# Performance work log

Hardware: AMD Instinct MI355X
Metric: run time of the kernel (lower is better)

Reference implementation:

```python
import jax, jax.numpy as jnp
import numpy as np

B, N, E, C_IN, C_OUT, N_LAYERS = 4, 20000, 16, 128, 128, 3


def setup_inputs() -> dict:
    key = jax.random.key(0)
    kx, ke, k0, k1, k2 = jax.random.split(key, 5)
    x = jax.random.normal(kx, (B, N, C_IN), dtype=jnp.float32)
    # neighbor lists padded with -1 (as in the torch module)
    edge_index = jax.random.randint(ke, (B, N, E), -1, N, dtype=jnp.int32)
    s_in = 1.0 / np.sqrt(C_IN)
    s_out = 1.0 / np.sqrt(C_OUT)
    W0 = jax.random.uniform(k0, (C_OUT, C_IN), minval=-s_in, maxval=s_in, dtype=jnp.float32)
    W1 = jax.random.uniform(k1, (C_OUT, C_OUT), minval=-s_out, maxval=s_out, dtype=jnp.float32)
    W2 = jax.random.uniform(k2, (C_OUT, C_OUT), minval=-s_out, maxval=s_out, dtype=jnp.float32)
    return {"x": x, "edge_index": edge_index, "W0": W0, "W1": W1, "W2": W2}


def gcn_layer(x, edge_index, W):
    # x: [B, N, Cin], edge_index: [B, N, E] (pad = -1), W: [Cout, Cin]
    n_nodes = x.shape[1]
    deg = jnp.sum(edge_index >= 0, axis=-1, keepdims=True).astype(x.dtype) + 1.0  # [B,N,1]
    inv_sqrt_deg = 1.0 / jnp.sqrt(deg)
    h = jnp.einsum('bnc,oc->bno', x, W) * inv_sqrt_deg  # transform + 1/sqrt(deg)
    # padding row of zeros at index n_nodes; map -1 -> n_nodes
    padded = jnp.concatenate(
        [h, jnp.zeros((h.shape[0], 1, h.shape[2]), h.dtype)], axis=1)  # [B,N+1,Cout]
    idx = jnp.where(edge_index < 0, n_nodes, edge_index)
    neigh = jax.vmap(lambda p, e: p[e])(padded, idx)  # [B,N,E,Cout] gather
    # sum over neighbors + self, then scale again by 1/sqrt(deg)
    return (jnp.sum(neigh, axis=-2) + h) * inv_sqrt_deg


def reference(x, edge_index, W0, W1, W2):
    for W in (W0, W1, W2):
        x = jax.nn.elu(gcn_layer(x, edge_index, W))
    return x
```

## Files before the change

### kernel.cpp

```cpp
#include <hip/hip_runtime.h>
#include <hip/hip_bf16.h>

#define NB 4
#define NN 20000
#define NE 16
#define NC 128
#define M_TOTAL (NB * NN)
#define BM 64

typedef __attribute__((ext_vector_type(8))) short bf16x8;
typedef __attribute__((ext_vector_type(4))) short short4v;
typedef __attribute__((ext_vector_type(4))) float f32x4;

static __device__ __forceinline__ short f2bf(float x) {
    __hip_bfloat16 h = __float2bfloat16(x);
    return *reinterpret_cast<short*>(&h);
}
static __device__ __forceinline__ float bf2f(short s) {
    __hip_bfloat16 h = *reinterpret_cast<__hip_bfloat16*>(&s);
    return __bfloat162float(h);
}

__global__ __launch_bounds__(256) void isd_kernel(const int* __restrict__ ei,
                                                  float* __restrict__ isd) {
    int g = blockIdx.x * 256 + threadIdx.x;
    if (g >= M_TOTAL) return;
    const int4* e4 = (const int4*)(ei + (size_t)g * NE);
    int cnt = 1;
#pragma unroll
    for (int q = 0; q < 4; ++q) {
        int4 v = e4[q];
        cnt += (v.x >= 0) + (v.y >= 0) + (v.z >= 0) + (v.w >= 0);
    }
    isd[g] = 1.0f / sqrtf((float)cnt);
}

__global__ __launch_bounds__(256) void wpack_kernel(const float* __restrict__ W,
                                                    short* __restrict__ wp) {
    const int id = blockIdx.x * 256 + threadIdx.x;
    const int s = id >> 9;
    const int f = (id >> 6) & 7;
    const int l = id & 63;
    const int o = f * 16 + (l & 15);
    const int kb = s * 32 + (l >> 4) * 8;
    const float4 v0 = *(const float4*)(W + (size_t)o * NC + kb);
    const float4 v1 = *(const float4*)(W + (size_t)o * NC + kb + 4);
    const float xs[8] = {v0.x, v0.y, v0.z, v0.w, v1.x, v1.y, v1.z, v1.w};
    bf16x8 hv, lv;
#pragma unroll
    for (int e = 0; e < 8; ++e) {
        const short h = f2bf(xs[e]);
        hv[e] = h;
        lv[e] = f2bf(xs[e] - bf2f(h));
    }
    short* dst = wp + (size_t)((s * 8 + f) * 2) * 512 + l * 8;
    *(bf16x8*)dst = hv;
    *(bf16x8*)(dst + 512) = lv;
}

__global__ __launch_bounds__(256) void matmul_kernel(const float* __restrict__ X,
                                                     const short* __restrict__ wp,
                                                     const float* __restrict__ isd,
                                                     float* __restrict__ H) {
    __shared__ short Ah[64 * 128];
    __shared__ short Al[64 * 128];
    const int t = threadIdx.x;
    const int bm = blockIdx.x * BM;

#pragma unroll
    for (int j = 0; j < 8; ++j) {
        const int fi = j * 256 + t;
        const int row = fi >> 5;
        const int k0 = (t & 31) * 4;
        const float4 v = *(const float4*)(X + (size_t)bm * NC + (size_t)fi * 4);
        const float xs[4] = {v.x, v.y, v.z, v.w};
        short4v hi, lo;
#pragma unroll
        for (int e = 0; e < 4; ++e) {
            const short h = f2bf(xs[e]);
            hi[e] = h;
            lo[e] = f2bf(xs[e] - bf2f(h));
        }
        const int kblk = k0 >> 3;
        const int dst = row * 128 + ((kblk ^ (row & 7)) << 3) + (k0 & 7);
        *(short4v*)(Ah + dst) = hi;
        *(short4v*)(Al + dst) = lo;
    }
    __syncthreads();

    const int w = t >> 6, l = t & 63;
    const int m0 = (w >> 1) * 32;
    const int oh = w & 1;
    const int lr = l & 15, lg = l >> 4;

    f32x4 acc[2][4];
#pragma unroll
    for (int mf = 0; mf < 2; ++mf)
#pragma unroll
        for (int fi = 0; fi < 4; ++fi) acc[mf][fi] = (f32x4){0.f, 0.f, 0.f, 0.f};

#pragma unroll
    for (int s = 0; s < 4; ++s) {
        bf16x8 a_h[2], a_l[2], b_h[4], b_l[4];
#pragma unroll
        for (int fi = 0; fi < 4; ++fi) {
            const int fg = oh * 4 + fi;
            const short* ph = wp + (size_t)((s * 8 + fg) * 2) * 512 + l * 8;
            b_h[fi] = *(const bf16x8*)ph;
            b_l[fi] = *(const bf16x8*)(ph + 512);
        }
#pragma unroll
        for (int mf = 0; mf < 2; ++mf) {
            const int row = m0 + mf * 16 + lr;
            const int kblk = (s * 4 + lg) ^ (l & 7);
            a_h[mf] = *(const bf16x8*)(Ah + row * 128 + kblk * 8);
            a_l[mf] = *(const bf16x8*)(Al + row * 128 + kblk * 8);
        }
#pragma unroll
        for (int mf = 0; mf < 2; ++mf)
#pragma unroll
            for (int fi = 0; fi < 4; ++fi) {
                acc[mf][fi] = __builtin_amdgcn_mfma_f32_16x16x32_bf16(
                    a_l[mf], b_h[fi], acc[mf][fi], 0, 0, 0);
                acc[mf][fi] = __builtin_amdgcn_mfma_f32_16x16x32_bf16(
                    a_h[mf], b_l[fi], acc[mf][fi], 0, 0, 0);
                acc[mf][fi] = __builtin_amdgcn_mfma_f32_16x16x32_bf16(
                    a_h[mf], b_h[fi], acc[mf][fi], 0, 0, 0);
            }
    }

#pragma unroll
    for (int mf = 0; mf < 2; ++mf)
#pragma unroll
        for (int r = 0; r < 4; ++r) {
            const int m = bm + m0 + mf * 16 + lg * 4 + r;
            const float sd = isd[m];
#pragma unroll
            for (int fi = 0; fi < 4; ++fi)
                H[(size_t)m * NC + oh * 64 + fi * 16 + lr] = acc[mf][fi][r] * sd;
        }
}

__global__ __launch_bounds__(256) void gather_kernel(const float* __restrict__ H,
                                                     const int* __restrict__ ei,
                                                     const float* __restrict__ isd,
                                                     float* __restrict__ out) {
    const int wid = threadIdx.x >> 6;
    const int lane = threadIdx.x & 63;
    int g = blockIdx.x * 4 + wid;
    g = __builtin_amdgcn_readfirstlane(g);
    const int base = (g / NN) * NN;

    const int4* e4 = (const int4*)(ei + (size_t)g * NE);
    const int4 ea = e4[0], eb = e4[1], ec = e4[2], ed = e4[3];
    const int e[NE] = {ea.x, ea.y, ea.z, ea.w, eb.x, eb.y, eb.z, eb.w,
                       ec.x, ec.y, ec.z, ec.w, ed.x, ed.y, ed.z, ed.w};

    const float2* h2 = (const float2*)H;
    float2 acc = h2[(size_t)g * 64 + lane];
#pragma unroll
    for (int q = 0; q < NE; ++q) {
        const int nbr = e[q];
        const int row = base + (nbr & ~(nbr >> 31));
        const float2 v = h2[(size_t)row * 64 + lane];
        if (nbr >= 0) { acc.x += v.x; acc.y += v.y; }
    }
    const float sd = isd[g];
    acc.x *= sd; acc.y *= sd;
    acc.x = acc.x > 0.0f ? acc.x : (__expf(acc.x) - 1.0f);
    acc.y = acc.y > 0.0f ? acc.y : (__expf(acc.y) - 1.0f);
    *(float2*)(out + (size_t)g * NC + (lane << 1)) = acc;
}

extern "C" void kernel_launch(void* const* d_in, const int* in_sizes, int n_in,
                              void* d_out, int out_size, void* d_ws, size_t ws_size,
                              hipStream_t stream) {
    const float* x = (const float*)d_in[0];
    const int* ei = (const int*)d_in[1];
    const float* W0 = (const float*)d_in[2];
    const float* W1 = (const float*)d_in[3];
    const float* W2 = (const float*)d_in[4];
    float* out = (float*)d_out;

    float* isd = (float*)d_ws;
    short* wp0 = (short*)((char*)d_ws + (320 << 10));
    short* wp1 = (short*)((char*)d_ws + (384 << 10));
    short* wp2 = (short*)((char*)d_ws + (448 << 10));
    float* h = (float*)((char*)d_ws + (512 << 10));

    isd_kernel<<<(M_TOTAL + 255) / 256, 256, 0, stream>>>(ei, isd);
    wpack_kernel<<<8, 256, 0, stream>>>(W0, wp0);
    wpack_kernel<<<8, 256, 0, stream>>>(W1, wp1);
    wpack_kernel<<<8, 256, 0, stream>>>(W2, wp2);

    matmul_kernel<<<M_TOTAL / BM, 256, 0, stream>>>(x, wp0, isd, h);
    gather_kernel<<<M_TOTAL / 4, 256, 0, stream>>>(h, ei, isd, out);
    matmul_kernel<<<M_TOTAL / BM, 256, 0, stream>>>(out, wp1, isd, h);
    gather_kernel<<<M_TOTAL / 4, 256, 0, stream>>>(h, ei, isd, out);
    matmul_kernel<<<M_TOTAL / BM, 256, 0, stream>>>(out, wp2, isd, h);
    gather_kernel<<<M_TOTAL / 4, 256, 0, stream>>>(h, ei, isd, out);
}
```

Before: 378.2 us.

## Emit bf16 hi/lo split from gather and DMA it into LDS in matmul

The gather epilogue of the first two layers now writes the activation already split into bf16 hi/lo halves, so the next matmul skips the fp32-to-bf16 split. That matmul loads the halves straight into LDS with global_load_lds, pre-swizzled. The gather also handles two nodes per wave with float4 loads and reads edge indices through lane shuffles, and the MFMA loop drops to unroll 2. The intermediate tiles reuse the output buffer, which trades the same byte count for less conversion work and fewer instructions.

Measured after the change: 376.8 us. About the same (-0.4%).

```diff
diff --git a/kernel.cpp b/kernel.cpp
--- a/kernel.cpp
+++ b/kernel.cpp
@@ -58,15 +58,56 @@
     *(bf16x8*)(dst + 512) = lv;
 }
 
-__global__ __launch_bounds__(256) void matmul_kernel(const float* __restrict__ X,
-                                                     const short* __restrict__ wp,
-                                                     const float* __restrict__ isd,
-                                                     float* __restrict__ H) {
+#define MFMA_PHASE(Ah, Al, wp, isd, H)                                          \
+    const int w = t >> 6, l = t & 63;                                           \
+    const int m0 = (w >> 1) * 32;                                               \
+    const int oh = w & 1;                                                       \
+    const int lr = l & 15, lg = l >> 4;                                         \
+    f32x4 acc[2][4];                                                            \
+    _Pragma("unroll") for (int mf = 0; mf < 2; ++mf)                            \
+        _Pragma("unroll") for (int fi = 0; fi < 4; ++fi)                        \
+            acc[mf][fi] = (f32x4){0.f, 0.f, 0.f, 0.f};                          \
+    _Pragma("unroll 2") for (int s = 0; s < 4; ++s) {                           \
+        bf16x8 a_h[2], a_l[2], b_h[4], b_l[4];                                  \
+        _Pragma("unroll") for (int fi = 0; fi < 4; ++fi) {                      \
+            const int fg = oh * 4 + fi;                                         \
+            const short* ph = wp + (size_t)((s * 8 + fg) * 2) * 512 + l * 8;    \
+            b_h[fi] = *(const bf16x8*)ph;                                       \
+            b_l[fi] = *(const bf16x8*)(ph + 512);                               \
+        }                                                                       \
+        _Pragma("unroll") for (int mf = 0; mf < 2; ++mf) {                      \
+            const int row = m0 + mf * 16 + lr;                                  \
+            const int kblk = (s * 4 + lg) ^ (l & 7);                            \
+            a_h[mf] = *(const bf16x8*)(Ah + row * 128 + kblk * 8);              \
+            a_l[mf] = *(const bf16x8*)(Al + row * 128 + kblk * 8);              \
+        }                                                                       \
+        _Pragma("unroll") for (int mf = 0; mf < 2; ++mf)                        \
+            _Pragma("unroll") for (int fi = 0; fi < 4; ++fi) {                  \
+                acc[mf][fi] = __builtin_amdgcn_mfma_f32_16x16x32_bf16(          \
+                    a_l[mf], b_h[fi], acc[mf][fi], 0, 0, 0);                    \
+                acc[mf][fi] = __builtin_amdgcn_mfma_f32_16x16x32_bf16(          \
+                    a_h[mf], b_l[fi], acc[mf][fi], 0, 0, 0);                    \
+                acc[mf][fi] = __builtin_amdgcn_mfma_f32_16x16x32_bf16(          \
+                    a_h[mf], b_h[fi], acc[mf][fi], 0, 0, 0);                    \
+            }                                                                   \
+    }                                                                           \
+    _Pragma("unroll") for (int mf = 0; mf < 2; ++mf)                            \
+        _Pragma("unroll") for (int r = 0; r < 4; ++r) {                         \
+            const int m = bm + m0 + mf * 16 + lg * 4 + r;                       \
+            const float sd = isd[m];                                            \
+            _Pragma("unroll") for (int fi = 0; fi < 4; ++fi)                    \
+                H[(size_t)m * NC + oh * 64 + fi * 16 + lr] =                    \
+                    acc[mf][fi][r] * sd;                                        \
+        }
+
+__global__ __launch_bounds__(256) void matmul_f32(const float* __restrict__ X,
+                                                  const short* __restrict__ wp,
+                                                  const float* __restrict__ isd,
+                                                  float* __restrict__ H) {
     __shared__ short Ah[64 * 128];
     __shared__ short Al[64 * 128];
     const int t = threadIdx.x;
     const int bm = blockIdx.x * BM;
-
 #pragma unroll
     for (int j = 0; j < 8; ++j) {
         const int fi = j * 256 + t;
@@ -87,89 +128,81 @@
         *(short4v*)(Al + dst) = lo;
     }
     __syncthreads();
-
+    MFMA_PHASE(Ah, Al, wp, isd, H)
+}
+
+__global__ __launch_bounds__(256) void matmul_split(const short* __restrict__ Xh,
+                                                    const short* __restrict__ Xl,
+                                                    const short* __restrict__ wp,
+                                                    const float* __restrict__ isd,
+                                                    float* __restrict__ H) {
+    __shared__ short Ah[64 * 128];
+    __shared__ short Al[64 * 128];
+    const int t = threadIdx.x;
+    const int bm = blockIdx.x * BM;
+    {
+        const int wv = t >> 6, ln = t & 63;
+        const int cbase0 = wv * 256;
+#pragma unroll
+        for (int i = 0; i < 4; ++i) {
+            const int cbase = cbase0 + i * 64;
+            const int cidx = cbase + ln;
+            const int r = cidx >> 4, sl = cidx & 15;
+            const int kg = sl ^ (r & 7);
+            const size_t goff = (size_t)(bm + r) * NC + kg * 8;
+            __builtin_amdgcn_global_load_lds(
+                (const __attribute__((address_space(1))) void*)(Xh + goff),
+                (__attribute__((address_space(3))) void*)(Ah + (size_t)cbase * 8),
+                16, 0, 0);
+            __builtin_amdgcn_global_load_lds(
+                (const __attribute__((address_space(1))) void*)(Xl + goff),
+                (__attribute__((address_space(3))) void*)(Al + (size_t)cbase * 8),
+                16, 0, 0);
+        }
+    }
+    __syncthreads();
+    MFMA_PHASE(Ah, Al, wp, isd, H)
+}
+
+template <bool SPLIT>
+__global__ __launch_bounds__(256) void gather2_kernel(
+    const float* __restrict__ H, const int* __restrict__ ei,
+    const float* __restrict__ isd, float* __restrict__ outf,
+    short* __restrict__ Xh, short* __restrict__ Xl) {
+    const int t = threadIdx.x;
     const int w = t >> 6, l = t & 63;
-    const int m0 = (w >> 1) * 32;
-    const int oh = w & 1;
-    const int lr = l & 15, lg = l >> 4;
-
-    f32x4 acc[2][4];
-#pragma unroll
-    for (int mf = 0; mf < 2; ++mf)
-#pragma unroll
-        for (int fi = 0; fi < 4; ++fi) acc[mf][fi] = (f32x4){0.f, 0.f, 0.f, 0.f};
-
-#pragma unroll
-    for (int s = 0; s < 4; ++s) {
-        bf16x8 a_h[2], a_l[2], b_h[4], b_l[4];
-#pragma unroll
-        for (int fi = 0; fi < 4; ++fi) {
-            const int fg = oh * 4 + fi;
-            const short* ph = wp + (size_t)((s * 8 + fg) * 2) * 512 + l * 8;
-            b_h[fi] = *(const bf16x8*)ph;
-            b_l[fi] = *(const bf16x8*)(ph + 512);
-        }
-#pragma unroll
-        for (int mf = 0; mf < 2; ++mf) {
-            const int row = m0 + mf * 16 + lr;
-            const int kblk = (s * 4 + lg) ^ (l & 7);
-            a_h[mf] = *(const bf16x8*)(Ah + row * 128 + kblk * 8);
-            a_l[mf] = *(const bf16x8*)(Al + row * 128 + kblk * 8);
-        }
-#pragma unroll
-        for (int mf = 0; mf < 2; ++mf)
-#pragma unroll
-            for (int fi = 0; fi < 4; ++fi) {
-                acc[mf][fi] = __builtin_amdgcn_mfma_f32_16x16x32_bf16(
-                    a_l[mf], b_h[fi], acc[mf][fi], 0, 0, 0);
-                acc[mf][fi] = __builtin_amdgcn_mfma_f32_16x16x32_bf16(
-                    a_h[mf], b_l[fi], acc[mf][fi], 0, 0, 0);
-                acc[mf][fi] = __builtin_amdgcn_mfma_f32_16x16x32_bf16(
-                    a_h[mf], b_h[fi], acc[mf][fi], 0, 0, 0);
-            }
-    }
-
-#pragma unroll
-    for (int mf = 0; mf < 2; ++mf)
-#pragma unroll
-        for (int r = 0; r < 4; ++r) {
-            const int m = bm + m0 + mf * 16 + lg * 4 + r;
-            const float sd = isd[m];
-#pragma unroll
-            for (int fi = 0; fi < 4; ++fi)
-                H[(size_t)m * NC + oh * 64 + fi * 16 + lr] = acc[mf][fi][r] * sd;
-        }
-}
-
-__global__ __launch_bounds__(256) void gather_kernel(const float* __restrict__ H,
-                                                     const int* __restrict__ ei,
-                                                     const float* __restrict__ isd,
-                                                     float* __restrict__ out) {
-    const int wid = threadIdx.x >> 6;
-    const int lane = threadIdx.x & 63;
-    int g = blockIdx.x * 4 + wid;
-    g = __builtin_amdgcn_readfirstlane(g);
-    const int base = (g / NN) * NN;
-
-    const int4* e4 = (const int4*)(ei + (size_t)g * NE);
-    const int4 ea = e4[0], eb = e4[1], ec = e4[2], ed = e4[3];
-    const int e[NE] = {ea.x, ea.y, ea.z, ea.w, eb.x, eb.y, eb.z, eb.w,
-                       ec.x, ec.y, ec.z, ec.w, ed.x, ed.y, ed.z, ed.w};
-
-    const float2* h2 = (const float2*)H;
-    float2 acc = h2[(size_t)g * 64 + lane];
+    const int g0 = blockIdx.x * 8 + w * 2;
+    const int gh = g0 + (l >> 5);
+    const int base = (g0 / NN) * NN;
+    const int ev = ei[(size_t)gh * NE + (l & 15)];
+    const float4* h4 = (const float4*)H;
+    const int c4 = l & 31;
+    float4 acc = h4[(size_t)gh * 32 + c4];
 #pragma unroll
     for (int q = 0; q < NE; ++q) {
-        const int nbr = e[q];
-        const int row = base + (nbr & ~(nbr >> 31));
-        const float2 v = h2[(size_t)row * 64 + lane];
-        if (nbr >= 0) { acc.x += v.x; acc.y += v.y; }
-    }
-    const float sd = isd[g];
-    acc.x *= sd; acc.y *= sd;
-    acc.x = acc.x > 0.0f ? acc.x : (__expf(acc.x) - 1.0f);
-    acc.y = acc.y > 0.0f ? acc.y : (__expf(acc.y) - 1.0f);
-    *(float2*)(out + (size_t)g * NC + (lane << 1)) = acc;
+        const int e = __shfl(ev, (l & 32) + q);
+        const int row = base + (e & ~(e >> 31));
+        const float4 v = h4[(size_t)row * 32 + c4];
+        if (e >= 0) { acc.x += v.x; acc.y += v.y; acc.z += v.z; acc.w += v.w; }
+    }
+    const float sd = isd[gh];
+    float o[4] = {acc.x * sd, acc.y * sd, acc.z * sd, acc.w * sd};
+#pragma unroll
+    for (int j = 0; j < 4; ++j) o[j] = o[j] > 0.f ? o[j] : (__expf(o[j]) - 1.f);
+    if (SPLIT) {
+        short4v hi, lo;
+#pragma unroll
+        for (int j = 0; j < 4; ++j) {
+            const short hb = f2bf(o[j]);
+            hi[j] = hb;
+            lo[j] = f2bf(o[j] - bf2f(hb));
+        }
+        *(short4v*)(Xh + (size_t)gh * NC + c4 * 4) = hi;
+        *(short4v*)(Xl + (size_t)gh * NC + c4 * 4) = lo;
+    } else {
+        float4 ov = {o[0], o[1], o[2], o[3]};
+        *(float4*)(outf + (size_t)gh * NC + c4 * 4) = ov;
+    }
 }
 
 extern "C" void kernel_launch(void* const* d_in, const int* in_sizes, int n_in,
@@ -188,15 +221,18 @@
     short* wp2 = (short*)((char*)d_ws + (448 << 10));
     float* h = (float*)((char*)d_ws + (512 << 10));
 
+    short* Xh = (short*)d_out;
+    short* Xl = Xh + (size_t)M_TOTAL * NC;
+
     isd_kernel<<<(M_TOTAL + 255) / 256, 256, 0, stream>>>(ei, isd);
     wpack_kernel<<<8, 256, 0, stream>>>(W0, wp0);
     wpack_kernel<<<8, 256, 0, stream>>>(W1, wp1);
     wpack_kernel<<<8, 256, 0, stream>>>(W2, wp2);
 
-    matmul_kernel<<<M_TOTAL / BM, 256, 0, stream>>>(x, wp0, isd, h);
-    gather_kernel<<<M_TOTAL / 4, 256, 0, stream>>>(h, ei, isd, out);
-    matmul_kernel<<<M_TOTAL / BM, 256, 0, stream>>>(out, wp1, isd, h);
-    gather_kernel<<<M_TOTAL / 4, 256, 0, stream>>>(h, ei, isd, out);
-    matmul_kernel<<<M_TOTAL / BM, 256, 0, stream>>>(out, wp2, isd, h);
-    gather_kernel<<<M_TOTAL / 4, 256, 0, stream>>>(h, ei, isd, out);
-}
+    matmul_f32<<<M_TOTAL / BM, 256, 0, stream>>>(x, wp0, isd, h);
+    gather2_kernel<true><<<M_TOTAL / 8, 256, 0, stream>>>(h, ei, isd, nullptr, Xh, Xl);
+    matmul_split<<<M_TOTAL / BM, 256, 0, stream>>>(Xh, Xl, wp1, isd, h);
+    gather2_kernel<true><<<M_TOTAL / 8, 256, 0, stream>>>(h, ei, isd, nullptr, Xh, Xl);
+    matmul_split<<<M_TOTAL / BM, 256, 0, stream>>>(Xh, Xl, wp2, isd, h);
+    gather2_kernel<false><<<M_TOTAL / 8, 256, 0, stream>>>(h, ei, isd, out, nullptr, nullptr);
+}
```
